# Kernel optimization log

Hardware: AMD Instinct MI355X
Metric: run time of the kernel (lower is better)

## Reference

```python
import jax, jax.numpy as jnp
import numpy as np

B, S, H = 1, 2048, 4096
NH, DN, DR, DV = 32, 128, 64, 128   # heads, nope dim, rope dim, v dim
QK = DN + DR                         # 192
RQ, RKV = 1536, 512
EPS = 1e-6
NEG = jnp.float32(-1e9)


def rmsnorm(x, w, eps=EPS):
    x32 = x.astype(jnp.float32)
    var = jnp.mean(x32 * x32, axis=-1, keepdims=True)
    return (x32 * jax.lax.rsqrt(var + eps)).astype(x.dtype) * w


def rope_complex(x, cos, sin):
    # x: [..., S, D]; interpret adjacent pairs as complex, multiply by e^{i*theta}
    xr, xi = x[..., 0::2], x[..., 1::2]
    or_ = xr * cos - xi * sin
    oi_ = xr * sin + xi * cos
    return jnp.stack([or_, oi_], axis=-1).reshape(x.shape)


def setup_inputs() -> dict:
    key = jax.random.key(0)
    ks = jax.random.split(key, 8)
    std = 0.02
    # RoPE angles: theta_j = pos * base^{-2j/DR}, shape [B, S, DR/2]
    inv_freq = 1.0 / (10000.0 ** (np.arange(0, DR, 2, dtype=np.float32) / DR))
    pos = np.arange(S, dtype=np.float32)
    freqs = jnp.asarray(np.broadcast_to(pos[:, None] * inv_freq[None, :], (B, S, DR // 2)))
    return {
        "hidden_states": jax.random.normal(ks[0], (B, S, H), jnp.float32),
        "freqs": freqs,
        "q_a_w": jax.random.normal(ks[1], (RQ, H), jnp.float32) * std,
        "q_a_ln_w": jnp.ones((RQ,), jnp.float32),
        "q_b_w": jax.random.normal(ks[2], (NH * QK, RQ), jnp.float32) * std,
        "kv_a_w": jax.random.normal(ks[3], (RKV + DR, H), jnp.float32) * std,
        "kv_a_ln_w": jnp.ones((RKV,), jnp.float32),
        "kv_b_w": jax.random.normal(ks[4], (NH * (DN + DV), RKV), jnp.float32) * std,
        "o_w": jax.random.normal(ks[5], (H, NH * DV), jnp.float32) * std,
    }


def reference(hidden_states, freqs, q_a_w, q_a_ln_w, q_b_w, kv_a_w, kv_a_ln_w, kv_b_w, o_w):
    b, s, _ = hidden_states.shape
    # --- low-rank Q: hidden -> q_lora_rank -> heads*(nope+rope) ---
    q = rmsnorm(hidden_states @ q_a_w.T, q_a_ln_w) @ q_b_w.T          # [B,S,NH*QK]
    q = q.reshape(b, s, NH, QK).transpose(0, 2, 1, 3)                  # [B,NH,S,QK]
    q_pass, q_rot = q[..., :DN], q[..., DN:]                           # [B,NH,S,DN],[B,NH,S,DR]
    # --- compressed KV + shared rope key ---
    ckv = hidden_states @ kv_a_w.T                                     # [B,S,RKV+DR]
    k_pass_c, k_rot = ckv[..., :RKV], ckv[..., RKV:]
    kv = rmsnorm(k_pass_c, kv_a_ln_w) @ kv_b_w.T                       # [B,S,NH*(DN+DV)]
    kv = kv.reshape(b, s, NH, DN + DV).transpose(0, 2, 1, 3)           # [B,NH,S,DN+DV]
    k_pass, v = kv[..., :DN], kv[..., DN:]
    k_rot = k_rot.reshape(b, 1, s, DR)                                 # [B,1,S,DR]
    # --- decoupled RoPE (complex form) ---
    cos = jnp.cos(freqs)[:, None]                                      # [B,1,S,DR/2]
    sin = jnp.sin(freqs)[:, None]
    q_rot = rope_complex(q_rot, cos, sin)
    k_rot = rope_complex(k_rot, cos, sin)
    k_rot = jnp.broadcast_to(k_rot, (b, NH, s, DR))
    query = jnp.concatenate([q_pass, q_rot], axis=-1)                  # [B,NH,S,QK]
    key = jnp.concatenate([k_pass, k_rot], axis=-1)
    # --- causal attention ---
    scaling = QK ** -0.5
    scores = jnp.einsum("bhqd,bhkd->bhqk", query, key) * scaling
    causal = jnp.tril(jnp.ones((s, s), bool))
    scores = jnp.where(causal, scores, NEG)
    probs = jax.nn.softmax(scores.astype(jnp.float32), axis=-1).astype(query.dtype)
    out = jnp.einsum("bhqk,bhkd->bhqd", probs, v)                      # [B,NH,S,DV]
    out = out.transpose(0, 2, 1, 3).reshape(b, s, NH * DV)
    return out @ o_w.T                                                 # [B,S,H]
```

## Files before the change

kernel.cpp:

```cpp
#include <hip/hip_runtime.h>
#define S_LEN 2048
#define HDIM 4096
#define NHEAD 32
#define QKD 192
#define RQ_ 1536
#define CKV_W 576
#define KVW 8192
#define QFW 6144
#define SC2F 0.1041216313667742f

typedef float f32x4 __attribute__((ext_vector_type(4)));
typedef __bf16 bf16x8 __attribute__((ext_vector_type(8)));

__device__ __forceinline__ unsigned short f2bf(float f) {
  unsigned int u = __float_as_uint(f);
  u += 0x7fffu + ((u >> 16) & 1u);
  return (unsigned short)(u >> 16);
}
__device__ __forceinline__ float b2f(unsigned short u) {
  return __uint_as_float((unsigned int)u << 16);
}
__device__ __forceinline__ float ex2(float x) { return exp2f(x); }

__device__ __forceinline__ void stage16(const void* g, void* lds_base, int lane) {
  __builtin_amdgcn_global_load_lds(
      (const __attribute__((address_space(1))) unsigned int*)g,
      (__attribute__((address_space(3))) unsigned int*)lds_base, 16, 0, 0);
}

__global__ __launch_bounds__(256) void cvt_kernel(
    const float* __restrict__ in, unsigned short* __restrict__ out, int n8) {
  int i = blockIdx.x * 256 + threadIdx.x;
  if (i >= n8) return;
  const float4* p = reinterpret_cast<const float4*>(in) + (size_t)i * 2;
  float4 a = p[0], b = p[1];
  unsigned long long lo = (unsigned long long)f2bf(a.x) | ((unsigned long long)f2bf(a.y) << 16)
      | ((unsigned long long)f2bf(a.z) << 32) | ((unsigned long long)f2bf(a.w) << 48);
  unsigned long long hi = (unsigned long long)f2bf(b.x) | ((unsigned long long)f2bf(b.y) << 16)
      | ((unsigned long long)f2bf(b.z) << 32) | ((unsigned long long)f2bf(b.w) << 48);
  unsigned long long* q = reinterpret_cast<unsigned long long*>(out) + (size_t)i * 2;
  q[0] = lo; q[1] = hi;
}

template<bool BF16OUT, bool SPLITK>
__global__ __launch_bounds__(256) void gemm_bf(
    const unsigned short* __restrict__ A, int lda,
    const unsigned short* __restrict__ B, int ldb,
    void* __restrict__ Cv, int ldc, int N, int K) {
  __shared__ unsigned short As[2][4][128][8];
  __shared__ unsigned short Bs[2][4][128][8];
  const int tid = threadIdx.x, lane = tid & 63, w = tid >> 6;
  const int gx = (int)gridDim.x, gy = (int)gridDim.y;
  const int nwg = gx * gy;
  int lin = (int)blockIdx.y * gx + (int)blockIdx.x;
  if ((nwg & 7) == 0) lin = (lin & 7) * (nwg >> 3) + (lin >> 3);
  const int bm = (lin % gy) * 128, bn = (lin / gy) * 128;
  const int koff = SPLITK ? (int)blockIdx.z * K : 0;
  const int wr = (w >> 1) * 64, wc = (w & 1) * 64;
  const int lg = lane >> 4, lm = lane & 15;
  f32x4 acc[4][4] = {};
  const int arow = bm + lane;
  int brow = bn + lane; if (brow >= N) brow = N - 1;

  auto STAGE = [&](int buf, int k0) {
#pragma unroll
    for (int i = 0; i < 2; ++i) {
      stage16(A + (size_t)(arow + i * 64) * lda + koff + k0 + w * 8, &As[buf][w][i * 64][0], lane);
      int br2 = brow + i * 64; if (br2 >= N) br2 = N - 1;
      stage16(B + (size_t)br2 * ldb + koff + k0 + w * 8, &Bs[buf][w][i * 64][0], lane);
    }
  };
  STAGE(0, 0);
  __syncthreads();
  int cur = 0;
  for (int k0 = 0; k0 < K; k0 += 32) {
    if (k0 + 32 < K) STAGE(cur ^ 1, k0 + 32);
    bf16x8 af[4], bf[4];
#pragma unroll
    for (int i = 0; i < 4; ++i)
      af[i] = *reinterpret_cast<const bf16x8*>(&As[cur][lg][wr + i * 16 + lm][0]);
#pragma unroll
    for (int j = 0; j < 4; ++j)
      bf[j] = *reinterpret_cast<const bf16x8*>(&Bs[cur][lg][wc + j * 16 + lm][0]);
    __builtin_amdgcn_s_setprio(1);
#pragma unroll
    for (int i = 0; i < 4; ++i)
#pragma unroll
      for (int j = 0; j < 4; ++j)
        acc[i][j] = __builtin_amdgcn_mfma_f32_16x16x32_bf16(af[i], bf[j], acc[i][j], 0, 0, 0);
    __builtin_amdgcn_s_setprio(0);
    __syncthreads();
    cur ^= 1;
  }
  size_t zoff = SPLITK ? (size_t)blockIdx.z * S_LEN * N : 0;
#pragma unroll
  for (int i = 0; i < 4; ++i)
#pragma unroll
    for (int j = 0; j < 4; ++j)
#pragma unroll
      for (int r = 0; r < 4; ++r) {
        int row = bm + wr + i * 16 + lg * 4 + r;
        int col = bn + wc + j * 16 + lm;
        if (col < N) {
          if constexpr (BF16OUT)
            ((unsigned short*)Cv)[(size_t)row * ldc + col] = f2bf(acc[i][j][r]);
          else
            ((float*)Cv)[zoff + (size_t)row * ldc + col] = acc[i][j][r];
        }
      }
}

__global__ __launch_bounds__(256) void rms_sum_q(
    const float* __restrict__ P, const float* __restrict__ w,
    unsigned short* __restrict__ y) {
  __shared__ float red[4];
  const int row = blockIdx.x, tid = threadIdx.x;
  const float* base = P + (size_t)row * RQ_;
  float x[6]; float ss = 0.f;
#pragma unroll
  for (int ii = 0; ii < 6; ++ii) {
    int j = tid + ii * 256;
    float v = 0.f;
#pragma unroll
    for (int z = 0; z < 4; ++z) v += base[(size_t)z * S_LEN * RQ_ + j];
    x[ii] = v; ss += v * v;
  }
#pragma unroll
  for (int off = 1; off < 64; off <<= 1) ss += __shfl_xor(ss, off, 64);
  if ((tid & 63) == 0) red[tid >> 6] = ss;
  __syncthreads();
  float scale = rsqrtf((red[0] + red[1] + red[2] + red[3]) / (float)RQ_ + 1e-6f);
  unsigned short* q = y + (size_t)row * RQ_;
#pragma unroll
  for (int ii = 0; ii < 6; ++ii) {
    int j = tid + ii * 256;
    q[j] = f2bf(x[ii] * scale * w[j]);
  }
}

__global__ __launch_bounds__(256) void rms_sum_kv(
    const float* __restrict__ P, const float* __restrict__ w,
    unsigned short* __restrict__ y, float* __restrict__ rotf) {
  __shared__ float red[4];
  const int row = blockIdx.x, tid = threadIdx.x;
  const float* base = P + (size_t)row * CKV_W;
  float x0 = 0.f, x1 = 0.f, x2 = 0.f;
#pragma unroll
  for (int z = 0; z < 8; ++z) {
    const float* b = base + (size_t)z * S_LEN * CKV_W;
    x0 += b[tid]; x1 += b[tid + 256];
    if (tid < 64) x2 += b[tid + 512];
  }
  float ss = x0 * x0 + x1 * x1;
#pragma unroll
  for (int off = 1; off < 64; off <<= 1) ss += __shfl_xor(ss, off, 64);
  if ((tid & 63) == 0) red[tid >> 6] = ss;
  __syncthreads();
  float scale = rsqrtf((red[0] + red[1] + red[2] + red[3]) / 512.0f + 1e-6f);
  unsigned short* q = y + (size_t)row * 512;
  q[tid] = f2bf(x0 * scale * w[tid]);
  q[tid + 256] = f2bf(x1 * scale * w[tid + 256]);
  if (tid < 64) rotf[(size_t)row * 64 + tid] = x2;
}

__global__ __launch_bounds__(256) void build_q_kernel(
    const unsigned short* __restrict__ qf, const float* __restrict__ freqs,
    unsigned short* __restrict__ Q) {
  int idx = blockIdx.x * 256 + threadIdx.x;
  if (idx >= NHEAD * S_LEN * 96) return;
  int j = idx % 96, s = (idx / 96) % S_LEN, h = idx / (96 * S_LEN);
  const unsigned short* src = qf + (size_t)s * QFW + h * QKD;
  unsigned int pk;
  if (j < 64) {
    pk = *reinterpret_cast<const unsigned int*>(&src[2 * j]);
  } else {
    int r = j - 64;
    float xr = b2f(src[128 + 2 * r]), xi = b2f(src[128 + 2 * r + 1]);
    float f = freqs[(size_t)s * 32 + r];
    float c = cosf(f), sn = sinf(f);
    pk = (unsigned int)f2bf(xr * c - xi * sn) | ((unsigned int)f2bf(xr * sn + xi * c) << 16);
  }
  *reinterpret_cast<unsigned int*>(Q + ((size_t)(h * S_LEN + s) * QKD + 2 * j)) = pk;
}

__global__ __launch_bounds__(256) void build_k_kernel(
    const unsigned short* __restrict__ kv, const float* __restrict__ rotf,
    const float* __restrict__ freqs, unsigned short* __restrict__ K) {
  int idx = blockIdx.x * 256 + threadIdx.x;
  if (idx >= NHEAD * S_LEN * 96) return;
  int j = idx % 96, s = (idx / 96) % S_LEN, h = idx / (96 * S_LEN);
  unsigned int pk;
  if (j < 64) {
    pk = *reinterpret_cast<const unsigned int*>(&kv[(size_t)s * KVW + h * 256 + 2 * j]);
  } else {
    int r = j - 64;
    float xr = rotf[(size_t)s * 64 + 2 * r];
    float xi = rotf[(size_t)s * 64 + 2 * r + 1];
    float f = freqs[(size_t)s * 32 + r];
    float c = cosf(f), sn = sinf(f);
    pk = (unsigned int)f2bf(xr * c - xi * sn) | ((unsigned int)f2bf(xr * sn + xi * c) << 16);
  }
  *reinterpret_cast<unsigned int*>(K + ((size_t)(h * S_LEN + s) * QKD + 2 * j)) = pk;
}

__global__ __launch_bounds__(256) void build_vt_kernel(
    const unsigned short* __restrict__ kv, unsigned short* __restrict__ Vt) {
  __shared__ unsigned short T[128][33];
  const int tid = threadIdx.x;
  const int h = blockIdx.y, s0 = blockIdx.x * 32;
#pragma unroll
  for (int p = 0; p < 16; ++p) {
    int i = p * 256 + tid;
    int d = i & 127, sr = i >> 7;
    T[d][sr] = kv[(size_t)(s0 + sr) * KVW + h * 256 + 128 + d];
  }
  __syncthreads();
#pragma unroll
  for (int p = 0; p < 8; ++p) {
    int i = p * 256 + tid;
    int d = i >> 4, sp = (i & 15) * 2;
    unsigned int pk = (unsigned int)T[d][sp] | ((unsigned int)T[d][sp + 1] << 16);
    *reinterpret_cast<unsigned int*>(Vt + (size_t)(h * 128 + d) * S_LEN + s0 + sp) = pk;
  }
}

__global__ __launch_bounds__(256, 3) void attn_kernel(
    const unsigned short* __restrict__ Q,
    const unsigned short* __restrict__ K,
    const unsigned short* __restrict__ Vt,
    unsigned short* __restrict__ O) {
  __shared__ unsigned short Ks[2][32 * 192];
  __shared__ unsigned short Vs[2][128 * 32];
  __shared__ unsigned short Ps[4][16 * 32];
  const int tid = threadIdx.x, lane = tid & 63, w = tid >> 6;
  const int wg = (int)blockIdx.x;
  const int lin = (wg & 7) * 128 + (wg >> 3);
  const int h = lin >> 5;
  const int qt = 31 - (lin & 31);
  const int qr0 = qt * 64 + w * 16;
  const int lg = lane >> 4, lm = lane & 15, lm7 = lane & 7;
  const unsigned short* Qh = Q + (size_t)h * S_LEN * QKD;
  const unsigned short* Kh = K + (size_t)h * S_LEN * QKD;
  const unsigned short* Vh = Vt + (size_t)h * 128 * S_LEN;

  bf16x8 qf[6];
#pragma unroll
  for (int f = 0; f < 6; ++f)
    qf[f] = *reinterpret_cast<const bf16x8*>(
        Qh + (size_t)(qr0 + lm) * QKD + f * 32 + lg * 8);

  f32x4 o[8] = {};
  float l[4] = {};

  auto STAGE = [&](int b, int kp) {
#pragma unroll
    for (int i = 0; i < 3; ++i) {
      int fb = (w * 3 + i) * 64 + lane;
      int row = fb / 24;
      int blk = fb - row * 24;
      int gb = (blk & ~7) | ((blk ^ row) & 7);
      stage16(Kh + (size_t)(kp + row) * QKD + gb * 8, &Ks[b][(w * 3 + i) * 512], lane);
    }
#pragma unroll
    for (int i = 0; i < 2; ++i) {
      int fb = (w * 2 + i) * 64 + lane;
      int row = fb >> 2;
      int blk = fb & 3;
      stage16(Vh + (size_t)row * S_LEN + kp + blk * 8, &Vs[b][(w * 2 + i) * 512], lane);
    }
  };

  const int ntiles = (qt + 1) * 2;
  STAGE(0, 0);
  __syncthreads();
  int buf = 0;
  for (int ti = 0; ti < ntiles; ++ti) {
    const int kp = ti * 32;
    if (ti + 1 < ntiles) STAGE(buf ^ 1, kp + 32);
    if (kp <= qr0 + 15) {
      f32x4 sc[2] = {};
      __builtin_amdgcn_s_setprio(1);
#pragma unroll
      for (int f = 0; f < 6; ++f)
#pragma unroll
        for (int c = 0; c < 2; ++c) {
          int blk = f * 4 + lg;
          int sb = (blk & ~7) | ((blk ^ lm7) & 7);
          bf16x8 kf = *reinterpret_cast<const bf16x8*>(&Ks[buf][(c * 16 + lm) * 192 + sb * 8]);
          sc[c] = __builtin_amdgcn_mfma_f32_16x16x32_bf16(qf[f], kf, sc[c], 0, 0, 0);
        }
      __builtin_amdgcn_s_setprio(0);
      const int rb = qr0 + lg * 4;
#pragma unroll
      for (int r = 0; r < 4; ++r) {
        const int row = rb + r;
        float v0 = fmaf(sc[0][r], SC2F, -32.f); if (kp + lm > row) v0 = -1e9f;
        float v1 = fmaf(sc[1][r], SC2F, -32.f); if (kp + 16 + lm > row) v1 = -1e9f;
        float p0 = ex2(v0), p1 = ex2(v1);
        l[r] += p0 + p1;
        int pr = lg * 4 + r;
        int s3 = pr & 3;
        int b0 = lm >> 3;
        unsigned short* pp = &Ps[w][pr * 32];
        pp[((b0 ^ s3) << 3) + lm7] = f2bf(p0);
        pp[(((2 + b0) ^ s3) << 3) + lm7] = f2bf(p1);
      }
      bf16x8 pa = *reinterpret_cast<const bf16x8*>(
          &Ps[w][lm * 32 + ((lg ^ (lm & 3)) << 3)]);
      __builtin_amdgcn_s_setprio(1);
#pragma unroll
      for (int d = 0; d < 8; ++d) {
        bf16x8 vf = *reinterpret_cast<const bf16x8*>(&Vs[buf][(d * 16 + lm) * 32 + lg * 8]);
        o[d] = __builtin_amdgcn_mfma_f32_16x16x32_bf16(pa, vf, o[d], 0, 0, 0);
      }
      __builtin_amdgcn_s_setprio(0);
    }
    __syncthreads();
    buf ^= 1;
  }
#pragma unroll
  for (int r = 0; r < 4; ++r) {
    float t = l[r];
#pragma unroll
    for (int off = 1; off < 16; off <<= 1) t += __shfl_xor(t, off, 16);
    float inv = 1.0f / t;
    int row = qr0 + lg * 4 + r;
#pragma unroll
    for (int d = 0; d < 8; ++d)
      O[(size_t)row * 4096 + h * 128 + d * 16 + lm] = f2bf(o[d][r] * inv);
  }
}

extern "C" void kernel_launch(void* const* d_in, const int* in_sizes, int n_in,
                              void* d_out, int out_size, void* d_ws, size_t ws_size,
                              hipStream_t stream) {
  const float* hs = (const float*)d_in[0];
  const float* freqs = (const float*)d_in[1];
  const float* q_a_w = (const float*)d_in[2];
  const float* q_a_ln = (const float*)d_in[3];
  const float* q_b_w = (const float*)d_in[4];
  const float* kv_a_w = (const float*)d_in[5];
  const float* kv_a_ln = (const float*)d_in[6];
  const float* kv_b_w = (const float*)d_in[7];
  const float* o_w = (const float*)d_in[8];
  float* out = (float*)d_out;

  char* ws = (char*)d_ws;
  unsigned short* wslot = (unsigned short*)(ws + 0);
  unsigned short* hs_bf = (unsigned short*)(ws + 33554432);
  unsigned short* attnb = (unsigned short*)(ws + 33554432);
  float* qa_part = (float*)(ws + 50331648);
  unsigned short* kv_bf = (unsigned short*)(ws + 50331648);
  float* ckv_part = (float*)(ws + 100663296);
  unsigned short* Qb = (unsigned short*)(ws + 100663296);
  unsigned short* qa_bf = (unsigned short*)(ws + 138412032);
  unsigned short* ckv_bf = (unsigned short*)(ws + 144703488);
  float* rotf = (float*)(ws + 146800640);
  unsigned short* qfullb = (unsigned short*)(ws + 147324928);
  unsigned short* Kb = (unsigned short*)(ws + 147324928);
  unsigned short* Vt = (unsigned short*)(ws + 172490752);

  dim3 blk(256);
  auto cvt = [&](const float* src, unsigned short* dst, size_t n) {
    int n8 = (int)(n / 8);
    cvt_kernel<<<(n8 + 255) / 256, blk, 0, stream>>>(src, dst, n8);
  };

  cvt(hs, hs_bf, (size_t)S_LEN * HDIM);
  cvt(q_a_w, wslot, (size_t)RQ_ * HDIM);
  gemm_bf<false, true><<<dim3(RQ_ / 128, S_LEN / 128, 4), blk, 0, stream>>>(
      hs_bf, HDIM, wslot, HDIM, qa_part, RQ_, RQ_, HDIM / 4);
  cvt(kv_a_w, wslot, (size_t)CKV_W * HDIM);
  gemm_bf<false, true><<<dim3((CKV_W + 127) / 128, S_LEN / 128, 8), blk, 0, stream>>>(
      hs_bf, HDIM, wslot, HDIM, ckv_part, CKV_W, CKV_W, HDIM / 8);
  rms_sum_q<<<S_LEN, blk, 0, stream>>>(qa_part, q_a_ln, qa_bf);
  rms_sum_kv<<<S_LEN, blk, 0, stream>>>(ckv_part, kv_a_ln, ckv_bf, rotf);
  cvt(q_b_w, wslot, (size_t)QFW * RQ_);
  gemm_bf<true, false><<<dim3(QFW / 128, S_LEN / 128), blk, 0, stream>>>(
      qa_bf, RQ_, wslot, RQ_, qfullb, QFW, QFW, RQ_);
  cvt(kv_b_w, wslot, (size_t)KVW * 512);
  gemm_bf<true, false><<<dim3(KVW / 128, S_LEN / 128), blk, 0, stream>>>(
      ckv_bf, 512, wslot, 512, kv_bf, KVW, KVW, 512);
  build_q_kernel<<<(NHEAD * S_LEN * 96 + 255) / 256, blk, 0, stream>>>(qfullb, freqs, Qb);
  build_k_kernel<<<(NHEAD * S_LEN * 96 + 255) / 256, blk, 0, stream>>>(kv_bf, rotf, freqs, Kb);
  build_vt_kernel<<<dim3(S_LEN / 32, NHEAD), blk, 0, stream>>>(kv_bf, Vt);
  attn_kernel<<<dim3(1024), blk, 0, stream>>>(Qb, Kb, Vt, attnb);
  cvt(o_w, wslot, (size_t)HDIM * HDIM);
  gemm_bf<false, false><<<dim3(HDIM / 128, S_LEN / 128), blk, 0, stream>>>(
      attnb, HDIM, wslot, HDIM, out, HDIM, HDIM, HDIM);
}
```

Measured before the change: 551.3 us.

## Fuse V transpose into kv_b GEMM epilogue and read Q/K in place

The kv_b GEMM now writes the V half of each head directly as transposed bf16 into Vt, which removes the separate transpose kernel. The Q and K build kernels are replaced: RoPE on Q is applied in place inside the full Q buffer, and the shared K rope part is computed once per position into a small buffer. The attention kernel reads Q and K_nope straight from the strided GEMM outputs and gathers the rope part from the shared buffer. This cuts several full-tensor copy passes, at the cost of strided loads in attention and scattered 8-byte writes in the GEMM epilogue.

Result: faster. 523.7 us (-5.0%).

```diff
diff --git a/kernel.cpp b/kernel.cpp
--- a/kernel.cpp
+++ b/kernel.cpp
@@ -42,11 +42,12 @@
   q[0] = lo; q[1] = hi;
 }
 
-template<bool BF16OUT, bool SPLITK>
+template<bool BF16OUT, bool SPLITK, bool VSCAT>
 __global__ __launch_bounds__(256) void gemm_bf(
     const unsigned short* __restrict__ A, int lda,
     const unsigned short* __restrict__ B, int ldb,
-    void* __restrict__ Cv, int ldc, int N, int K) {
+    void* __restrict__ Cv, int ldc, int N, int K,
+    unsigned short* __restrict__ VtOut) {
   __shared__ unsigned short As[2][4][128][8];
   __shared__ unsigned short Bs[2][4][128][8];
   const int tid = threadIdx.x, lane = tid & 63, w = tid >> 6;
@@ -92,6 +93,27 @@
     __syncthreads();
     cur ^= 1;
   }
+
+  if constexpr (VSCAT) {
+    if (bn & 128) {
+      const int h2 = bn >> 8;
+#pragma unroll
+      for (int i = 0; i < 4; ++i)
+#pragma unroll
+        for (int j = 0; j < 4; ++j) {
+          int d = wc + j * 16 + lm;
+          unsigned long long pk =
+                (unsigned long long)f2bf(acc[i][j][0])
+              | ((unsigned long long)f2bf(acc[i][j][1]) << 16)
+              | ((unsigned long long)f2bf(acc[i][j][2]) << 32)
+              | ((unsigned long long)f2bf(acc[i][j][3]) << 48);
+          *reinterpret_cast<unsigned long long*>(
+              VtOut + (size_t)(h2 * 128 + d) * S_LEN + bm + wr + i * 16 + lg * 4) = pk;
+        }
+      return;
+    }
+  }
+
   size_t zoff = SPLITK ? (size_t)blockIdx.z * S_LEN * N : 0;
 #pragma unroll
   for (int i = 0; i < 4; ++i)
@@ -163,70 +185,37 @@
   if (tid < 64) rotf[(size_t)row * 64 + tid] = x2;
 }
 
-__global__ __launch_bounds__(256) void build_q_kernel(
-    const unsigned short* __restrict__ qf, const float* __restrict__ freqs,
-    unsigned short* __restrict__ Q) {
+__global__ __launch_bounds__(256) void rope_q_kernel(
+    unsigned short* __restrict__ qf, const float* __restrict__ freqs) {
   int idx = blockIdx.x * 256 + threadIdx.x;
-  if (idx >= NHEAD * S_LEN * 96) return;
-  int j = idx % 96, s = (idx / 96) % S_LEN, h = idx / (96 * S_LEN);
-  const unsigned short* src = qf + (size_t)s * QFW + h * QKD;
-  unsigned int pk;
-  if (j < 64) {
-    pk = *reinterpret_cast<const unsigned int*>(&src[2 * j]);
-  } else {
-    int r = j - 64;
-    float xr = b2f(src[128 + 2 * r]), xi = b2f(src[128 + 2 * r + 1]);
-    float f = freqs[(size_t)s * 32 + r];
-    float c = cosf(f), sn = sinf(f);
-    pk = (unsigned int)f2bf(xr * c - xi * sn) | ((unsigned int)f2bf(xr * sn + xi * c) << 16);
-  }
-  *reinterpret_cast<unsigned int*>(Q + ((size_t)(h * S_LEN + s) * QKD + 2 * j)) = pk;
-}
-
-__global__ __launch_bounds__(256) void build_k_kernel(
-    const unsigned short* __restrict__ kv, const float* __restrict__ rotf,
-    const float* __restrict__ freqs, unsigned short* __restrict__ K) {
+  if (idx >= NHEAD * S_LEN * 32) return;
+  int r = idx & 31, s = (idx >> 5) & (S_LEN - 1), h = idx >> 16;
+  unsigned short* p = qf + (size_t)s * QFW + h * QKD + 128 + 2 * r;
+  float xr = b2f(p[0]), xi = b2f(p[1]);
+  float f = freqs[(size_t)s * 32 + r];
+  float c = cosf(f), sn = sinf(f);
+  *reinterpret_cast<unsigned int*>(p) =
+      (unsigned int)f2bf(xr * c - xi * sn) | ((unsigned int)f2bf(xr * sn + xi * c) << 16);
+}
+
+__global__ __launch_bounds__(256) void rope_k_kernel(
+    const float* __restrict__ rotf, const float* __restrict__ freqs,
+    unsigned short* __restrict__ Kr) {
   int idx = blockIdx.x * 256 + threadIdx.x;
-  if (idx >= NHEAD * S_LEN * 96) return;
-  int j = idx % 96, s = (idx / 96) % S_LEN, h = idx / (96 * S_LEN);
-  unsigned int pk;
-  if (j < 64) {
-    pk = *reinterpret_cast<const unsigned int*>(&kv[(size_t)s * KVW + h * 256 + 2 * j]);
-  } else {
-    int r = j - 64;
-    float xr = rotf[(size_t)s * 64 + 2 * r];
-    float xi = rotf[(size_t)s * 64 + 2 * r + 1];
-    float f = freqs[(size_t)s * 32 + r];
-    float c = cosf(f), sn = sinf(f);
-    pk = (unsigned int)f2bf(xr * c - xi * sn) | ((unsigned int)f2bf(xr * sn + xi * c) << 16);
-  }
-  *reinterpret_cast<unsigned int*>(K + ((size_t)(h * S_LEN + s) * QKD + 2 * j)) = pk;
-}
-
-__global__ __launch_bounds__(256) void build_vt_kernel(
-    const unsigned short* __restrict__ kv, unsigned short* __restrict__ Vt) {
-  __shared__ unsigned short T[128][33];
-  const int tid = threadIdx.x;
-  const int h = blockIdx.y, s0 = blockIdx.x * 32;
-#pragma unroll
-  for (int p = 0; p < 16; ++p) {
-    int i = p * 256 + tid;
-    int d = i & 127, sr = i >> 7;
-    T[d][sr] = kv[(size_t)(s0 + sr) * KVW + h * 256 + 128 + d];
-  }
-  __syncthreads();
-#pragma unroll
-  for (int p = 0; p < 8; ++p) {
-    int i = p * 256 + tid;
-    int d = i >> 4, sp = (i & 15) * 2;
-    unsigned int pk = (unsigned int)T[d][sp] | ((unsigned int)T[d][sp + 1] << 16);
-    *reinterpret_cast<unsigned int*>(Vt + (size_t)(h * 128 + d) * S_LEN + s0 + sp) = pk;
-  }
+  if (idx >= S_LEN * 32) return;
+  int r = idx & 31, s = idx >> 5;
+  float xr = rotf[(size_t)s * 64 + 2 * r];
+  float xi = rotf[(size_t)s * 64 + 2 * r + 1];
+  float f = freqs[(size_t)s * 32 + r];
+  float c = cosf(f), sn = sinf(f);
+  *reinterpret_cast<unsigned int*>(Kr + (size_t)s * 64 + 2 * r) =
+      (unsigned int)f2bf(xr * c - xi * sn) | ((unsigned int)f2bf(xr * sn + xi * c) << 16);
 }
 
 __global__ __launch_bounds__(256, 3) void attn_kernel(
-    const unsigned short* __restrict__ Q,
-    const unsigned short* __restrict__ K,
+    const unsigned short* __restrict__ Qf,
+    const unsigned short* __restrict__ KV,
+    const unsigned short* __restrict__ Kr,
     const unsigned short* __restrict__ Vt,
     unsigned short* __restrict__ O) {
   __shared__ unsigned short Ks[2][32 * 192];
@@ -239,15 +228,15 @@
   const int qt = 31 - (lin & 31);
   const int qr0 = qt * 64 + w * 16;
   const int lg = lane >> 4, lm = lane & 15, lm7 = lane & 7;
-  const unsigned short* Qh = Q + (size_t)h * S_LEN * QKD;
-  const unsigned short* Kh = K + (size_t)h * S_LEN * QKD;
+  const unsigned short* Qh = Qf + h * QKD;
+  const int hoff = h * 256;
   const unsigned short* Vh = Vt + (size_t)h * 128 * S_LEN;
 
   bf16x8 qf[6];
 #pragma unroll
   for (int f = 0; f < 6; ++f)
     qf[f] = *reinterpret_cast<const bf16x8*>(
-        Qh + (size_t)(qr0 + lm) * QKD + f * 32 + lg * 8);
+        Qh + (size_t)(qr0 + lm) * QFW + f * 32 + lg * 8);
 
   f32x4 o[8] = {};
   float l[4] = {};
@@ -259,7 +248,10 @@
       int row = fb / 24;
       int blk = fb - row * 24;
       int gb = (blk & ~7) | ((blk ^ row) & 7);
-      stage16(Kh + (size_t)(kp + row) * QKD + gb * 8, &Ks[b][(w * 3 + i) * 512], lane);
+      const unsigned short* src = (blk < 16)
+          ? KV + (size_t)(kp + row) * KVW + hoff + gb * 8
+          : Kr + (size_t)(kp + row) * 64 + (gb - 16) * 8;
+      stage16(src, &Ks[b][(w * 3 + i) * 512], lane);
     }
 #pragma unroll
     for (int i = 0; i < 2; ++i) {
@@ -352,13 +344,12 @@
   float* qa_part = (float*)(ws + 50331648);
   unsigned short* kv_bf = (unsigned short*)(ws + 50331648);
   float* ckv_part = (float*)(ws + 100663296);
-  unsigned short* Qb = (unsigned short*)(ws + 100663296);
   unsigned short* qa_bf = (unsigned short*)(ws + 138412032);
   unsigned short* ckv_bf = (unsigned short*)(ws + 144703488);
   float* rotf = (float*)(ws + 146800640);
   unsigned short* qfullb = (unsigned short*)(ws + 147324928);
-  unsigned short* Kb = (unsigned short*)(ws + 147324928);
   unsigned short* Vt = (unsigned short*)(ws + 172490752);
+  unsigned short* Kr = (unsigned short*)(ws + 189267968);
 
   dim3 blk(256);
   auto cvt = [&](const float* src, unsigned short* dst, size_t n) {
@@ -368,24 +359,23 @@
 
   cvt(hs, hs_bf, (size_t)S_LEN * HDIM);
   cvt(q_a_w, wslot, (size_t)RQ_ * HDIM);
-  gemm_bf<false, true><<<dim3(RQ_ / 128, S_LEN / 128, 4), blk, 0, stream>>>(
-      hs_bf, HDIM, wslot, HDIM, qa_part, RQ_, RQ_, HDIM / 4);
+  gemm_bf<false, true, false><<<dim3(RQ_ / 128, S_LEN / 128, 4), blk, 0, stream>>>(
+      hs_bf, HDIM, wslot, HDIM, qa_part, RQ_, RQ_, HDIM / 4, nullptr);
   cvt(kv_a_w, wslot, (size_t)CKV_W * HDIM);
-  gemm_bf<false, true><<<dim3((CKV_W + 127) / 128, S_LEN / 128, 8), blk, 0, stream>>>(
-      hs_bf, HDIM, wslot, HDIM, ckv_part, CKV_W, CKV_W, HDIM / 8);
+  gemm_bf<false, true, false><<<dim3((CKV_W + 127) / 128, S_LEN / 128, 8), blk, 0, stream>>>(
+      hs_bf, HDIM, wslot, HDIM, ckv_part, CKV_W, CKV_W, HDIM / 8, nullptr);
   rms_sum_q<<<S_LEN, blk, 0, stream>>>(qa_part, q_a_ln, qa_bf);
   rms_sum_kv<<<S_LEN, blk, 0, stream>>>(ckv_part, kv_a_ln, ckv_bf, rotf);
   cvt(q_b_w, wslot, (size_t)QFW * RQ_);
-  gemm_bf<true, false><<<dim3(QFW / 128, S_LEN / 128), blk, 0, stream>>>(
-      qa_bf, RQ_, wslot, RQ_, qfullb, QFW, QFW, RQ_);
+  gemm_bf<true, false, false><<<dim3(QFW / 128, S_LEN / 128), blk, 0, stream>>>(
+      qa_bf, RQ_, wslot, RQ_, qfullb, QFW, QFW, RQ_, nullptr);
   cvt(kv_b_w, wslot, (size_t)KVW * 512);
-  gemm_bf<true, false><<<dim3(KVW / 128, S_LEN / 128), blk, 0, stream>>>(
-      ckv_bf, 512, wslot, 512, kv_bf, KVW, KVW, 512);
-  build_q_kernel<<<(NHEAD * S_LEN * 96 + 255) / 256, blk, 0, stream>>>(qfullb, freqs, Qb);
-  build_k_kernel<<<(NHEAD * S_LEN * 96 + 255) / 256, blk, 0, stream>>>(kv_bf, rotf, freqs, Kb);
-  build_vt_kernel<<<dim3(S_LEN / 32, NHEAD), blk, 0, stream>>>(kv_bf, Vt);
-  attn_kernel<<<dim3(1024), blk, 0, stream>>>(Qb, Kb, Vt, attnb);
+  gemm_bf<true, false, true><<<dim3(KVW / 128, S_LEN / 128), blk, 0, stream>>>(
+      ckv_bf, 512, wslot, 512, kv_bf, KVW, KVW, 512, Vt);
+  rope_q_kernel<<<(NHEAD * S_LEN * 32 + 255) / 256, blk, 0, stream>>>(qfullb, freqs);
+  rope_k_kernel<<<(S_LEN * 32 + 255) / 256, blk, 0, stream>>>(rotf, freqs, Kr);
+  attn_kernel<<<dim3(1024), blk, 0, stream>>>(qfullb, kv_bf, Kr, Vt, attnb);
   cvt(o_w, wslot, (size_t)HDIM * HDIM);
-  gemm_bf<false, false><<<dim3(HDIM / 128, S_LEN / 128), blk, 0, stream>>>(
-      attnb, HDIM, wslot, HDIM, out, HDIM, HDIM, HDIM);
-}
+  gemm_bf<false, false, false><<<dim3(HDIM / 128, S_LEN / 128), blk, 0, stream>>>(
+      attnb, HDIM, wslot, HDIM, out, HDIM, HDIM, HDIM, nullptr);
+}
```
